# Optimization experiments

Measured on AMD Instinct MI355X. Metric: run time of the kernel, lower is better.

## Reference

```python
import jax, jax.numpy as jnp
import numpy as np

B = 1024        # sessions
N = 32          # nodes per session
S = 50          # steps per session
H = 256         # hidden_size
V = 50000       # vocab size of embedding_table
GROUP = 3       # items pooled per step (reshape(-1, 3, H) in source)
SAN_BLOCKS = 3


def setup_inputs() -> dict:
    key = jax.random.key(0)
    ks = jax.random.split(key, 16)
    node_embedding = jax.random.normal(ks[0], (B * N, H), jnp.float32)
    emb_weight = jax.random.normal(ks[1], (V, H), jnp.float32) * 0.02
    batch = jnp.repeat(jnp.arange(B, dtype=jnp.int32), N)           # session id per node
    sequence = jax.random.randint(ks[2], (B * S, GROUP), 0, N + 1)  # local idx; ==N -> zero pad row
    itemset_len = jax.random.randint(ks[3], (B * S,), 1, GROUP + 1).astype(jnp.float32)
    sequence_len = jnp.full((B,), S, dtype=jnp.int32)               # steps per session
    cue = jax.random.randint(ks[4], (B,), 0, V)
    sc = 1.0 / np.sqrt(H)
    in_proj_w = jax.random.normal(ks[5], (3 * H, H), jnp.float32) * sc
    in_proj_b = jnp.zeros((3 * H,), jnp.float32)
    out_proj_w = jax.random.normal(ks[6], (H, H), jnp.float32) * sc
    out_proj_b = jnp.zeros((H,), jnp.float32)
    d1_w = jax.random.normal(ks[7], (H, H), jnp.float32) * sc
    d1_b = jnp.zeros((H,), jnp.float32)
    d2_w = jax.random.normal(ks[8], (H, H), jnp.float32) * sc
    d2_b = jnp.zeros((H,), jnp.float32)
    W3_w = jax.random.normal(ks[9], (H, 2 * H), jnp.float32) * (1.0 / np.sqrt(2 * H))
    W3_b = jnp.zeros((H,), jnp.float32)
    return {
        "node_embedding": node_embedding, "emb_weight": emb_weight,
        "itemset_len": itemset_len, "in_proj_w": in_proj_w, "in_proj_b": in_proj_b,
        "out_proj_w": out_proj_w, "out_proj_b": out_proj_b,
        "d1_w": d1_w, "d1_b": d1_b, "d2_w": d2_w, "d2_b": d2_b,
        "W3_w": W3_w, "W3_b": W3_b,
        "batch": batch, "sequence": sequence, "sequence_len": sequence_len, "cue": cue,
    }


def reference(node_embedding, emb_weight, itemset_len, in_proj_w, in_proj_b,
              out_proj_w, out_proj_b, d1_w, d1_b, d2_w, d2_b, W3_w, W3_b,
              batch, sequence, sequence_len, cue):
    # Eval mode: dropout disabled.
    total_nodes, h = node_embedding.shape
    nsess = sequence_len.shape[0]
    total_steps = sequence.shape[0]

    # Per-session node counts and exclusive offsets (replaces torch.split on ragged batch).
    sections = jnp.bincount(batch, length=nsess)
    offsets = jnp.cumsum(sections) - sections

    # Append one global zero row; local index == sections[sess] maps to it
    # (matches the per-session zero row in v_i_zeros).
    nodes_pad = jnp.concatenate([node_embedding, jnp.zeros((1, h), node_embedding.dtype)], axis=0)
    step_sess = jnp.repeat(jnp.arange(nsess), sequence_len, total_repeat_length=total_steps)
    sec_s = sections[step_sess][:, None]
    off_s = offsets[step_sess][:, None]
    gidx = jnp.where(sequence == sec_s, total_nodes, off_s + sequence)  # [T, 3] global indices

    # session_i: 3-way sum of gathered node embeddings / itemset_len  -> [T, H]
    step_emb = nodes_pad[gidx].sum(axis=1) / itemset_len[:, None]

    # Last step of each session (both v_n and the position s_g is read from).
    last_idx = jnp.cumsum(sequence_len) - 1
    v_n = step_emb[last_idx]  # [B, H]

    # nn.MultiheadAttention receives (L=1, N=steps, E=H): softmax over a single key
    # is identically 1, so MHA == out_proj(v_proj(x)) applied per step independently.
    # Hence the SAN chain on the last step equals the chain applied to v_n alone.
    Wv = in_proj_w[2 * h:]
    bv = in_proj_b[2 * h:]
    x = v_n
    for _ in range(SAN_BLOCKS):
        attn = (x @ Wv.T + bv) @ out_proj_w.T + out_proj_b
        # Residual FFN (dropout off in eval): x + d2(relu(d1(x)))
        x = attn + (jax.nn.relu(attn @ d1_w.T + d1_b) @ d2_w.T + d2_b)
    s_g = x  # [B, H]

    s_h = jnp.concatenate([v_n, s_g], axis=1) @ W3_w.T + W3_b  # [B, H]
    y_hat = jnp.sum(s_h * emb_weight[cue], axis=1)             # [B]
    all_scores = s_h @ emb_weight.T                            # [B, V]
    return y_hat, all_scores
```

## Files before the change

### kernel.cpp

```cpp
#include <hip/hip_runtime.h>
#include <hip/hip_bf16.h>
#include <stdint.h>

typedef __attribute__((ext_vector_type(8))) short short8;
typedef __attribute__((ext_vector_type(4))) short short4v;
typedef __attribute__((ext_vector_type(4))) float f32x4;

#define HD 256

__device__ __forceinline__ ushort f2bf(float f) {
  union { float f; uint32_t u; } x; x.f = f;
  uint32_t r = (x.u + 0x7fffu + ((x.u >> 16) & 1u)) >> 16;
  return (ushort)r;
}

__device__ __forceinline__ int swz(int row, int col) {
  int chunk = (col >> 3) ^ (row & 7);
  return row * 256 + chunk * 8 + (col & 7);
}

__global__ void prep1_kernel(const float* __restrict__ in_proj_w,
                             const float* __restrict__ in_proj_b,
                             const float* __restrict__ out_proj_w,
                             const float* __restrict__ out_proj_b,
                             const float* __restrict__ d1_w,
                             const float* __restrict__ d2_w,
                             const float* __restrict__ W3_w,
                             ushort* __restrict__ Wc_bf, ushort* __restrict__ d1_bf,
                             ushort* __restrict__ d2_bf, ushort* __restrict__ W3_bf,
                             float* __restrict__ bc) {
  int blk = blockIdx.x, t = threadIdx.x;
  if (blk < 256) {
    int i = blk * 256 + t;
    d1_bf[i] = f2bf(d1_w[i]);
    d2_bf[i] = f2bf(d2_w[i]);
    W3_bf[i] = f2bf(W3_w[i]);
    W3_bf[i + 65536] = f2bf(W3_w[i + 65536]);
  } else {
    int i = blk - 256;
    const float* Po = out_proj_w + i * HD;
    const float* Wv = in_proj_w + 2 * HD * HD;
    float acc = 0.f;
    for (int m = 0; m < HD; ++m) acc += Po[m] * Wv[m * HD + t];
    Wc_bf[i * HD + t] = f2bf(acc);
    if (t == 0) {
      const float* bv = in_proj_b + 2 * HD;
      float b = out_proj_b[i];
      for (int m = 0; m < HD; ++m) b += Po[m] * bv[m];
      bc[i] = b;
    }
  }
}

__global__ void scan_kernel(const int* __restrict__ batch, int total_nodes,
                            const int* __restrict__ seq_len,
                            int* __restrict__ sections, int* __restrict__ offsets,
                            int* __restrict__ last_idx, int nsess) {
  __shared__ int lbs[1025];
  __shared__ int s2[1024];
  int t = threadIdx.x;
  if (t < nsess) {
    int lo = 0, hi = total_nodes;
    while (lo < hi) {
      int mid = (lo + hi) >> 1;
      if (batch[mid] < t) lo = mid + 1; else hi = mid;
    }
    lbs[t] = lo;
  }
  if (t == 0) lbs[nsess] = total_nodes;
  int v2 = (t < nsess) ? seq_len[t] : 0;
  s2[t] = v2;
  for (int d = 1; d < 1024; d <<= 1) {
    __syncthreads();
    int a2 = (t >= d) ? s2[t - d] : 0;
    __syncthreads();
    s2[t] += a2;
  }
  __syncthreads();
  if (t < nsess) {
    offsets[t] = lbs[t];
    sections[t] = lbs[t + 1] - lbs[t];
    last_idx[t] = s2[t] - 1;
  }
}

template<bool RELU, bool RESID, bool WACC>
__device__ __forceinline__ void gemm_stage16(const ushort* inA, const ushort* __restrict__ Wbf,
                                             const float* __restrict__ bias,
                                             float* accf, ushort* outB) {
  int t = threadIdx.x;
  int lane = t & 63, wid = t >> 6;
  int la = lane & 15, g = lane >> 4;
  int col = wid * 16 + la;
  f32x4 acc0 = {0.f, 0.f, 0.f, 0.f};
  f32x4 acc1 = {0.f, 0.f, 0.f, 0.f};
#pragma unroll
  for (int kk = 0; kk < 4; ++kk) {
    short8 a0 = *(const short8*)&inA[swz(la, kk * 32 + g * 8)];
    short8 b0 = *(const short8*)&Wbf[col * HD + kk * 32 + g * 8];
    short8 a1 = *(const short8*)&inA[swz(la, (kk + 4) * 32 + g * 8)];
    short8 b1 = *(const short8*)&Wbf[col * HD + (kk + 4) * 32 + g * 8];
    acc0 = __builtin_amdgcn_mfma_f32_16x16x32_bf16(a0, b0, acc0, 0, 0, 0);
    acc1 = __builtin_amdgcn_mfma_f32_16x16x32_bf16(a1, b1, acc1, 0, 0, 0);
  }
  float bia = bias[col];
#pragma unroll
  for (int r = 0; r < 4; ++r) {
    int ro = g * 4 + r;
    float v = acc0[r] + acc1[r] + bia;
    if (RELU) v = fmaxf(v, 0.f);
    if (RESID) v += accf[ro * HD + col];
    if (WACC) accf[ro * HD + col] = v;
    outB[swz(ro, col)] = f2bf(v);
  }
}

__device__ __forceinline__ void stage_fence() {
  __syncthreads();
  __builtin_amdgcn_sched_barrier(0);
}

__global__ __launch_bounds__(1024, 1) void sh_kernel(
    const float* __restrict__ node_emb, const float* __restrict__ emb_w,
    const float* __restrict__ itemset_len,
    const float* __restrict__ d1_b, const float* __restrict__ d2_b,
    const float* __restrict__ W3_b, const float* __restrict__ bc,
    const int* __restrict__ sequence, const int* __restrict__ cue,
    const int* __restrict__ sections, const int* __restrict__ offsets,
    const int* __restrict__ last_idx,
    const ushort* __restrict__ Wc_bf, const ushort* __restrict__ d1_bf,
    const ushort* __restrict__ d2_bf, const ushort* __restrict__ W3_bf,
    ushort* __restrict__ sh_bf, float* __restrict__ y_hat, int group) {
  __shared__ float accf[16 * HD];
  __shared__ ushort vn_bf[16 * HD];
  __shared__ ushort bufA[16 * HD];
  __shared__ ushort bufB[16 * HD];
  int t = threadIdx.x;
  int b0 = blockIdx.x * 16;

  {
    int r = t >> 6, cg = t & 63;
    int sess = b0 + r;
    int li = last_idx[sess];
    float inv = 1.0f / itemset_len[li];
    int sec = sections[sess], off = offsets[sess];
    float4 s = {0.f, 0.f, 0.f, 0.f};
    for (int gi = 0; gi < group; ++gi) {
      int sq = sequence[li * group + gi];
      if (sq == sec) continue;
      float4 v = *(const float4*)(node_emb + (size_t)(off + sq) * HD + cg * 4);
      s.x += v.x; s.y += v.y; s.z += v.z; s.w += v.w;
    }
    short4v u;
    u[0] = (short)f2bf(s.x * inv); u[1] = (short)f2bf(s.y * inv);
    u[2] = (short)f2bf(s.z * inv); u[3] = (short)f2bf(s.w * inv);
    *(short4v*)&vn_bf[swz(r, cg * 4)] = u;
  }
  stage_fence();

  const ushort* x = vn_bf;
  ushort* P = bufA;
  ushort* Q = bufB;
#pragma unroll 1
  for (int sb = 0; sb < 3; ++sb) {
    gemm_stage16<false, false, true>(x, Wc_bf, bc, accf, P);
    stage_fence();
    gemm_stage16<true, false, false>(P, d1_bf, d1_b, nullptr, Q);
    stage_fence();
    gemm_stage16<false, true, false>(Q, d2_bf, d2_b, accf, P);
    stage_fence();
    x = P;
    ushort* tmp = P; P = Q; Q = tmp;
  }

  {
    int lane = t & 63, wid = t >> 6;
    int la = lane & 15, g = lane >> 4;
    int col = wid * 16 + la;
    f32x4 acc0 = {0.f, 0.f, 0.f, 0.f};
    f32x4 acc1 = {0.f, 0.f, 0.f, 0.f};
#pragma unroll
    for (int kk = 0; kk < 8; ++kk) {
      short8 a0 = *(const short8*)&vn_bf[swz(la, kk * 32 + g * 8)];
      short8 b0 = *(const short8*)&W3_bf[col * 2 * HD + kk * 32 + g * 8];
      short8 a1 = *(const short8*)&x[swz(la, kk * 32 + g * 8)];
      short8 b1 = *(const short8*)&W3_bf[col * 2 * HD + (kk + 8) * 32 + g * 8];
      acc0 = __builtin_amdgcn_mfma_f32_16x16x32_bf16(a0, b0, acc0, 0, 0, 0);
      acc1 = __builtin_amdgcn_mfma_f32_16x16x32_bf16(a1, b1, acc1, 0, 0, 0);
    }
    float bia = W3_b[col];
#pragma unroll
    for (int r = 0; r < 4; ++r) {
      int ro = g * 4 + r;
      float v = acc0[r] + acc1[r] + bia;
      accf[ro * HD + col] = v;
      sh_bf[(size_t)(b0 + ro) * HD + col] = f2bf(v);
    }
  }
  stage_fence();

  {
    int r = t >> 6, lane = t & 63;
    const float4 er = *(const float4*)(emb_w + (size_t)cue[b0 + r] * HD + lane * 4);
    const float* ar = &accf[r * HD + lane * 4];
    float p = ar[0] * er.x + ar[1] * er.y + ar[2] * er.z + ar[3] * er.w;
#pragma unroll
    for (int off = 32; off >= 1; off >>= 1) p += __shfl_down(p, off, 64);
    if (lane == 0) y_hat[b0 + r] = p;
  }
}

__global__ __launch_bounds__(256, 2) void score_kernel(
    const ushort* __restrict__ sh_bf, const float* __restrict__ emb_w,
    float* __restrict__ scores, int nrows, int V) {
  __shared__ ushort ebuf[64 * HD];
  __shared__ float obuf[64][65];
  int t = threadIdx.x;
  int c0 = blockIdx.x * 64;
#pragma unroll
  for (int i = 0; i < 8; ++i) {
    int c = t + i * 256;
    int row = c >> 5, q = c & 31;
    if (c0 + row < V) {
      const float4* src = (const float4*)(emb_w + (size_t)(c0 + row) * HD + q * 8);
      float4 v0 = src[0], v1 = src[1];
      short8 u;
      u[0] = (short)f2bf(v0.x); u[1] = (short)f2bf(v0.y);
      u[2] = (short)f2bf(v0.z); u[3] = (short)f2bf(v0.w);
      u[4] = (short)f2bf(v1.x); u[5] = (short)f2bf(v1.y);
      u[6] = (short)f2bf(v1.z); u[7] = (short)f2bf(v1.w);
      *(short8*)&ebuf[row * 256 + ((q ^ (row & 7)) * 8)] = u;
    }
  }
  __syncthreads();

  int lane = t & 63, wid = t >> 6;
  int la = lane & 15, g = lane >> 4;
  short8 bfr[32];
#pragma unroll
  for (int kk = 0; kk < 8; ++kk)
#pragma unroll
    for (int ct = 0; ct < 4; ++ct) {
      int brow = ct * 16 + la;
      bfr[kk * 4 + ct] = *(const short8*)&ebuf[brow * 256 + (((kk * 4 + g) ^ (brow & 7)) * 8)];
    }

  int nrb = nrows >> 6;
  int cg = c0 + lane;
  bool cok = cg < V;
  for (int rb = 0; rb < nrb; ++rb) {
    int r0 = rb * 64 + wid * 16;
    const ushort* arow = sh_bf + (size_t)(r0 + la) * HD;
    short8 a[8];
#pragma unroll
    for (int kk = 0; kk < 8; ++kk) a[kk] = *(const short8*)&arow[kk * 32 + g * 8];
    f32x4 acc[4] = {{0.f,0.f,0.f,0.f},{0.f,0.f,0.f,0.f},{0.f,0.f,0.f,0.f},{0.f,0.f,0.f,0.f}};
#pragma unroll
    for (int kk = 0; kk < 8; ++kk) {
#pragma unroll
      for (int ct = 0; ct < 4; ++ct)
        acc[ct] = __builtin_amdgcn_mfma_f32_16x16x32_bf16(a[kk], bfr[kk * 4 + ct], acc[ct], 0, 0, 0);
    }
#pragma unroll
    for (int ct = 0; ct < 4; ++ct)
#pragma unroll
      for (int r = 0; r < 4; ++r)
        obuf[wid * 16 + g * 4 + r][ct * 16 + la] = acc[ct][r];
#pragma unroll
    for (int i = 0; i < 16; ++i) {
      int row = wid * 16 + i;
      float v = obuf[row][lane];
      if (cok)
        __builtin_nontemporal_store(v, &scores[(size_t)(rb * 64 + row) * V + cg]);
    }
  }
}

extern "C" void kernel_launch(void* const* d_in, const int* in_sizes, int n_in,
                              void* d_out, int out_size, void* d_ws, size_t ws_size,
                              hipStream_t stream) {
  const float* node_emb   = (const float*)d_in[0];
  const float* emb_w      = (const float*)d_in[1];
  const float* itemset_len= (const float*)d_in[2];
  const float* in_proj_w  = (const float*)d_in[3];
  const float* in_proj_b  = (const float*)d_in[4];
  const float* out_proj_w = (const float*)d_in[5];
  const float* out_proj_b = (const float*)d_in[6];
  const float* d1_w       = (const float*)d_in[7];
  const float* d1_b       = (const float*)d_in[8];
  const float* d2_w       = (const float*)d_in[9];
  const float* d2_b       = (const float*)d_in[10];
  const float* W3_w       = (const float*)d_in[11];
  const float* W3_b       = (const float*)d_in[12];
  const int*   batch      = (const int*)d_in[13];
  const int*   sequence   = (const int*)d_in[14];
  const int*   seq_len    = (const int*)d_in[15];
  const int*   cue        = (const int*)d_in[16];

  int total_nodes = in_sizes[0] / HD;
  int V           = in_sizes[1] / HD;
  int nsess       = in_sizes[15];
  int total_steps = in_sizes[2];
  int group       = in_sizes[14] / total_steps;

  char* ws = (char*)d_ws;
  int* sections   = (int*)(ws);
  int* offsets    = (int*)(ws + 4096);
  int* last_idx   = (int*)(ws + 8192);
  float* bc       = (float*)(ws + 12288);
  ushort* sh_bf   = (ushort*)(ws + 16384);
  ushort* Wc_bf   = (ushort*)(ws + 16384 + 524288);
  ushort* d1_bf   = Wc_bf + HD * HD;
  ushort* d2_bf   = d1_bf + HD * HD;
  ushort* W3_bf   = d2_bf + HD * HD;

  float* y_hat  = (float*)d_out;
  float* scores = (float*)d_out + nsess;

  prep1_kernel<<<512, 256, 0, stream>>>(in_proj_w, in_proj_b, out_proj_w, out_proj_b,
                                        d1_w, d2_w, W3_w,
                                        Wc_bf, d1_bf, d2_bf, W3_bf, bc);
  scan_kernel<<<1, 1024, 0, stream>>>(batch, total_nodes, seq_len,
                                      sections, offsets, last_idx, nsess);
  sh_kernel<<<nsess / 16, 1024, 0, stream>>>(node_emb, emb_w, itemset_len,
                                             d1_b, d2_b, W3_b, bc,
                                             sequence, cue, sections, offsets, last_idx,
                                             Wc_bf, d1_bf, d2_bf, W3_bf,
                                             sh_bf, y_hat, group);
  score_kernel<<<(V + 63) / 64, 256, 0, stream>>>(sh_bf, emb_w, scores, nsess, V);
}
```

Baseline: 136.3 us.

## Pre-pack embedding table into bf16 MFMA fragments and widen score tiles

```diff
diff --git a/kernel.cpp b/kernel.cpp
--- a/kernel.cpp
+++ b/kernel.cpp
@@ -26,8 +26,10 @@
                              const float* __restrict__ d1_w,
                              const float* __restrict__ d2_w,
                              const float* __restrict__ W3_w,
+                             const float* __restrict__ emb_w, int V,
                              ushort* __restrict__ Wc_bf, ushort* __restrict__ d1_bf,
                              ushort* __restrict__ d2_bf, ushort* __restrict__ W3_bf,
+                             ushort* __restrict__ ebf_t,
                              float* __restrict__ bc) {
   int blk = blockIdx.x, t = threadIdx.x;
   if (blk < 256) {
@@ -36,7 +38,7 @@
     d2_bf[i] = f2bf(d2_w[i]);
     W3_bf[i] = f2bf(W3_w[i]);
     W3_bf[i + 65536] = f2bf(W3_w[i + 65536]);
-  } else {
+  } else if (blk < 512) {
     int i = blk - 256;
     const float* Po = out_proj_w + i * HD;
     const float* Wv = in_proj_w + 2 * HD * HD;
@@ -48,6 +50,22 @@
       float b = out_proj_b[i];
       for (int m = 0; m < HD; ++m) b += Po[m] * bv[m];
       bc[i] = b;
+    }
+  } else {
+    int s = blk - 512;
+#pragma unroll
+    for (int i = 0; i < 8; ++i) {
+      int idx = t + i * 256;
+      int j = idx >> 6, lane = idx & 63;
+      int ct = j & 3, kk = j >> 2, la = lane & 15, g = lane >> 4;
+      int row = s * 64 + ct * 16 + la;
+      short8 u = {0, 0, 0, 0, 0, 0, 0, 0};
+      if (row < V) {
+        const float* src = emb_w + (size_t)row * HD + kk * 32 + g * 8;
+#pragma unroll
+        for (int e = 0; e < 8; ++e) u[e] = (short)f2bf(src[e]);
+      }
+      *(short8*)&ebf_t[((size_t)(s * 32 + j) * 64 + lane) * 8] = u;
     }
   }
 }
@@ -211,68 +229,54 @@
 }
 
 __global__ __launch_bounds__(256, 2) void score_kernel(
-    const ushort* __restrict__ sh_bf, const float* __restrict__ emb_w,
+    const ushort* __restrict__ sh_bf, const ushort* __restrict__ ebf_t,
     float* __restrict__ scores, int nrows, int V) {
-  __shared__ ushort ebuf[64 * HD];
-  __shared__ float obuf[64][65];
+  __shared__ float obuf[64][264];
   int t = threadIdx.x;
-  int c0 = blockIdx.x * 64;
-#pragma unroll
-  for (int i = 0; i < 8; ++i) {
-    int c = t + i * 256;
-    int row = c >> 5, q = c & 31;
-    if (c0 + row < V) {
-      const float4* src = (const float4*)(emb_w + (size_t)(c0 + row) * HD + q * 8);
-      float4 v0 = src[0], v1 = src[1];
-      short8 u;
-      u[0] = (short)f2bf(v0.x); u[1] = (short)f2bf(v0.y);
-      u[2] = (short)f2bf(v0.z); u[3] = (short)f2bf(v0.w);
-      u[4] = (short)f2bf(v1.x); u[5] = (short)f2bf(v1.y);
-      u[6] = (short)f2bf(v1.z); u[7] = (short)f2bf(v1.w);
-      *(short8*)&ebuf[row * 256 + ((q ^ (row & 7)) * 8)] = u;
-    }
-  }
-  __syncthreads();
-
   int lane = t & 63, wid = t >> 6;
   int la = lane & 15, g = lane >> 4;
+  int c0 = blockIdx.x * 256;
+  int strip = blockIdx.x * 4 + wid;
+
+  const ushort* tb = ebf_t + (size_t)strip * 32 * 64 * 8;
   short8 bfr[32];
 #pragma unroll
-  for (int kk = 0; kk < 8; ++kk)
-#pragma unroll
-    for (int ct = 0; ct < 4; ++ct) {
-      int brow = ct * 16 + la;
-      bfr[kk * 4 + ct] = *(const short8*)&ebuf[brow * 256 + (((kk * 4 + g) ^ (brow & 7)) * 8)];
-    }
+  for (int j = 0; j < 32; ++j)
+    bfr[j] = *(const short8*)&tb[(j * 64 + lane) * 8];
 
   int nrb = nrows >> 6;
-  int cg = c0 + lane;
-  bool cok = cg < V;
+  bool cok = (c0 + lane * 4 + 4) <= V;
   for (int rb = 0; rb < nrb; ++rb) {
-    int r0 = rb * 64 + wid * 16;
-    const ushort* arow = sh_bf + (size_t)(r0 + la) * HD;
-    short8 a[8];
-#pragma unroll
-    for (int kk = 0; kk < 8; ++kk) a[kk] = *(const short8*)&arow[kk * 32 + g * 8];
-    f32x4 acc[4] = {{0.f,0.f,0.f,0.f},{0.f,0.f,0.f,0.f},{0.f,0.f,0.f,0.f},{0.f,0.f,0.f,0.f}};
-#pragma unroll
-    for (int kk = 0; kk < 8; ++kk) {
+    int r0 = rb * 64;
+#pragma unroll
+    for (int sg = 0; sg < 4; ++sg) {
+      const ushort* arow = sh_bf + (size_t)(r0 + sg * 16 + la) * HD;
+      short8 a[8];
+#pragma unroll
+      for (int kk = 0; kk < 8; ++kk) a[kk] = *(const short8*)&arow[kk * 32 + g * 8];
+      f32x4 acc[4] = {{0.f,0.f,0.f,0.f},{0.f,0.f,0.f,0.f},{0.f,0.f,0.f,0.f},{0.f,0.f,0.f,0.f}};
+#pragma unroll
+      for (int kk = 0; kk < 8; ++kk) {
+#pragma unroll
+        for (int ct = 0; ct < 4; ++ct)
+          acc[ct] = __builtin_amdgcn_mfma_f32_16x16x32_bf16(a[kk], bfr[kk * 4 + ct], acc[ct], 0, 0, 0);
+      }
 #pragma unroll
       for (int ct = 0; ct < 4; ++ct)
-        acc[ct] = __builtin_amdgcn_mfma_f32_16x16x32_bf16(a[kk], bfr[kk * 4 + ct], acc[ct], 0, 0, 0);
-    }
-#pragma unroll
-    for (int ct = 0; ct < 4; ++ct)
-#pragma unroll
-      for (int r = 0; r < 4; ++r)
-        obuf[wid * 16 + g * 4 + r][ct * 16 + la] = acc[ct][r];
+#pragma unroll
+        for (int r = 0; r < 4; ++r)
+          obuf[sg * 16 + g * 4 + r][wid * 64 + ct * 16 + la] = acc[ct][r];
+    }
+    __syncthreads();
 #pragma unroll
     for (int i = 0; i < 16; ++i) {
       int row = wid * 16 + i;
-      float v = obuf[row][lane];
+      f32x4 v = *(const f32x4*)&obuf[row][lane * 4];
       if (cok)
-        __builtin_nontemporal_store(v, &scores[(size_t)(rb * 64 + row) * V + cg]);
-    }
+        __builtin_nontemporal_store(
+            v, (f32x4*)&scores[(size_t)(r0 + row) * V + c0 + lane * 4]);
+    }
+    __syncthreads();
   }
 }
 
@@ -303,6 +307,9 @@
   int total_steps = in_sizes[2];
   int group       = in_sizes[14] / total_steps;
 
+  int nblk  = (V + 255) / 256;
+  int nstrip = nblk * 4;
+
   char* ws = (char*)d_ws;
   int* sections   = (int*)(ws);
   int* offsets    = (int*)(ws + 4096);
@@ -313,13 +320,14 @@
   ushort* d1_bf   = Wc_bf + HD * HD;
   ushort* d2_bf   = d1_bf + HD * HD;
   ushort* W3_bf   = d2_bf + HD * HD;
+  ushort* ebf_t   = (ushort*)(ws + 2097152);
 
   float* y_hat  = (float*)d_out;
   float* scores = (float*)d_out + nsess;
 
-  prep1_kernel<<<512, 256, 0, stream>>>(in_proj_w, in_proj_b, out_proj_w, out_proj_b,
-                                        d1_w, d2_w, W3_w,
-                                        Wc_bf, d1_bf, d2_bf, W3_bf, bc);
+  prep1_kernel<<<512 + nstrip, 256, 0, stream>>>(
+      in_proj_w, in_proj_b, out_proj_w, out_proj_b, d1_w, d2_w, W3_w,
+      emb_w, V, Wc_bf, d1_bf, d2_bf, W3_bf, ebf_t, bc);
   scan_kernel<<<1, 1024, 0, stream>>>(batch, total_nodes, seq_len,
                                       sections, offsets, last_idx, nsess);
   sh_kernel<<<nsess / 16, 1024, 0, stream>>>(node_emb, emb_w, itemset_len,
@@ -327,5 +335,5 @@
                                              sequence, cue, sections, offsets, last_idx,
                                              Wc_bf, d1_bf, d2_bf, W3_bf,
                                              sh_bf, y_hat, group);
-  score_kernel<<<(V + 63) / 64, 256, 0, stream>>>(sh_bf, emb_w, scores, nsess, V);
-}
+  score_kernel<<<nblk, 256, 0, stream>>>(sh_bf, ebf_t, scores, nsess, V);
+}
```

Measured after the change: 150.6 us. 10.5% more time.
